# Performance work log

Measured on AMD Instinct MI355X. Metric: run time of the kernel, lower is better.

## Reference

```python
import jax, jax.numpy as jnp
import numpy as np

ALPHA = 1.0
NEG = -1e20  # boundary value used by the torch module


def _compute_mu(W, alpha):
    """DTW location parameter mu: [B, Na+1, Nb+1].
    mu[i,j] = alpha*W[i-1,j-1] + logsumexp(mu[i-1,j], mu[i,j-1], mu[i-1,j-1]).
    Row-wise scan (outer over i) with an inner scan over j for the
    left-dependency; fully vectorized over batch.
    """
    B, Na, Nb = W.shape
    aW = alpha * W  # [B, Na, Nb]
    # row 0: mu[:,0,0]=0, mu[:,0,1:]=-1e20
    row0 = jnp.concatenate([jnp.zeros((B, 1), W.dtype),
                            jnp.full((B, Nb), NEG, W.dtype)], axis=1)

    def row_step(prev_row, w_row):  # prev_row [B, Nb+1], w_row [B, Nb]
        up = prev_row[:, 1:]    # mu[i-1, j]   for j=1..Nb -> [B, Nb]
        diag = prev_row[:, :-1]  # mu[i-1, j-1]            -> [B, Nb]

        def col_step(left, inp):
            u, d, w = inp  # each [B]
            val = w + jax.nn.logsumexp(jnp.stack([u, left, d], axis=0), axis=0)
            return val, val

        left0 = jnp.full((B,), NEG, W.dtype)  # mu[i, 0] = -1e20
        xs = (up.T, diag.T, w_row.T)          # scan over Nb
        _, vals = jax.lax.scan(col_step, left0, xs)  # [Nb, B]
        new_row = jnp.concatenate([jnp.full((B, 1), NEG, W.dtype), vals.T], axis=1)
        return new_row, new_row

    _, rows = jax.lax.scan(row_step, row0, jnp.swapaxes(aW, 0, 1))  # [Na, B, Nb+1]
    mu = jnp.concatenate([row0[:, None, :], jnp.swapaxes(rows, 0, 1)], axis=1)
    return mu  # [B, Na+1, Nb+1]


def _compute_pi(W, mu, mask, alpha):
    """Reduced transition tensor pi: [B, Na, Nb, 3] (softmax over moves)."""
    up = mu[:, :-1, 1:]    # mu[i-1, j]
    left = mu[:, 1:, :-1]  # mu[i, j-1]
    diag = mu[:, :-1, :-1]  # mu[i-1, j-1]
    raw = jnp.stack([up, left, diag], axis=-1) + alpha * W[..., None]
    return jax.nn.softmax(raw, axis=-1) * mask


def setup_inputs() -> dict:
    key = jax.random.key(0)
    k1, _ = jax.random.split(key)
    B, Na, Nb = 64, 384, 384
    W = jax.random.normal(k1, (B, Na, Nb), dtype=jnp.float32)
    mask = jnp.ones((B, Na, Nb, 1), dtype=jnp.float32)
    return {"W": W, "mask": mask}


def reference(W, mask):
    mu = _compute_mu(W, ALPHA)
    pi = _compute_pi(W, mu, mask, ALPHA)
    return (mu, pi)
```

## Files before the change

### kernel.cpp

```cpp
#include <hip/hip_runtime.h>

#define NA 384
#define NB 384
#define NBATCH 64
#define NEGV -1e20f
#define C 8
#define NCW 6
#define TOT_CH 56
#define WPITCH 68
#define LOG2E 1.44269504088896340736f
#define LN2   0.69314718055994530942f

typedef float f4 __attribute__((ext_vector_type(4)));

struct alignas(16) SharedT {
    float stage[2][NCW][64 * 9];
    float wtile[4][NCW][8 * WPITCH];
    float bound[NCW - 1][NB + 1];
    int   progress[NCW - 1];
    int   computed[NCW];
    int   drained[NCW][2];
    int   wready[NCW];
};

__device__ __forceinline__ void loadW8(const float* __restrict__ Wb, int rbase,
                                       int kk, int l, float (&r)[8])
{
    const int rl = l >> 3, cc = l & 7;
    const int colb = 8 * kk + cc;
#pragma unroll
    for (int i = 0; i < 8; ++i) {
        const int row = 8 * i + rl;
        int col = colb - row;
        col = col < 0 ? 0 : (col > NB - 1 ? NB - 1 : col);
        r[i] = Wb[(size_t)(rbase + row) * NB + col];
    }
}

__device__ __forceinline__ void writeWt(float* __restrict__ wt,
                                        const float (&r)[8], int l) {
#pragma unroll
    for (int i = 0; i < 8; ++i) wt[i * WPITCH + l] = r[i];
}

__device__ __forceinline__ void readWc(const float* __restrict__ wt, int l,
                                       float (&wc)[8]) {
    const int wb = (l >> 3) * WPITCH + (l & 7) * 8;
    const f4 lo = *(const f4*)(wt + wb);
    const f4 hi = *(const f4*)(wt + wb + 4);
    wc[0] = lo.x * LOG2E; wc[1] = lo.y * LOG2E;
    wc[2] = lo.z * LOG2E; wc[3] = lo.w * LOG2E;
    wc[4] = hi.x * LOG2E; wc[5] = hi.y * LOG2E;
    wc[6] = hi.z * LOG2E; wc[7] = hi.w * LOG2E;
}

template<bool FULL>
__device__ __forceinline__ void chunk_body(int k, int w, int l,
        float (&wc)[8], float& val, float& diag, SharedT& sh)
{
    const int s0 = 1 + k * C;

    if (k >= 2) {
        volatile int* dr = &sh.drained[w][k & 1];
        while (*dr < k - 2) __builtin_amdgcn_s_sleep(1);
        __builtin_amdgcn_sched_barrier(0);
        asm volatile("" ::: "memory");
    }
    if (w > 0 && s0 <= NB) {
        const int need = (s0 + C - 1 < NB) ? s0 + C - 1 : NB;
        volatile int* pr = &sh.progress[w - 1];
        while (*pr < need) { }
        __builtin_amdgcn_sched_barrier(0);
        asm volatile("" ::: "memory");
    }
    float bnd[C];
    if (w > 0) {
#pragma unroll
        for (int c = 0; c < C; ++c) {
            const int s = s0 + c;
            bnd[c] = sh.bound[w - 1][s <= NB ? s : NB];
        }
    }

    float* st = &sh.stage[k & 1][w][0];
    __builtin_amdgcn_s_setprio(1);
#pragma unroll
    for (int c = 0; c < C; ++c) {
        const int s = s0 + c;
        float upv = __int_as_float(__builtin_amdgcn_update_dpp(
            0, __float_as_int(val), 0x138 , 0xF, 0xF, false));
        if (l == 0) upv = (w > 0 && s <= NB) ? bnd[c] : NEGV;
        const int j = s - l;
        if (FULL || (j >= 1 && j <= NB)) {
            const float m  = fmaxf(fmaxf(upv, val), diag);
            const float eu = exp2f(upv  - m);
            const float el = exp2f(val  - m);
            const float ed = exp2f(diag - m);
            const float nv = wc[c] + m + __log2f(eu + el + ed);
            st[l * 9 + c] = nv;
            if (w < NCW - 1 && l == 63) sh.bound[w][j] = nv;
            diag = upv;
            val  = nv;
        }
    }
    asm volatile("s_waitcnt lgkmcnt(0)" ::: "memory");
    if (l == 63) {
        if (w < NCW - 1) {
            const int done = s0 + C - 1 - 63;
            if (done >= 1) *(volatile int*)&sh.progress[w] = done;
        }
        *(volatile int*)&sh.computed[w] = k + 1;
    }
    __builtin_amdgcn_s_setprio(0);

    if (k + 1 < TOT_CH) {
        volatile int* wr = &sh.wready[w];
        while (*wr < k + 2) { }
        __builtin_amdgcn_sched_barrier(0);
        asm volatile("" ::: "memory");
        readWc(&sh.wtile[(k + 1) & 3][w][0], l, wc);
    }
}

template<bool FULL>
__device__ __forceinline__ void io_iter(int k, int cw, int l,
        const float* __restrict__ Wb, int rbase, float* __restrict__ mub,
        float (&wreg)[8], SharedT& sh)
{
    volatile int* cp = &sh.computed[cw];
    while (*cp < k + 1) __builtin_amdgcn_s_sleep(1);
    __builtin_amdgcn_sched_barrier(0);
    asm volatile("" ::: "memory");

    const float* st = &sh.stage[k & 1][cw][0];
    float v[8];
    const int lr = l >> 3, cc = l & 7;
#pragma unroll
    for (int q = 0; q < 8; ++q) v[q] = st[(lr + 8 * q) * 9 + cc];
    asm volatile("s_waitcnt lgkmcnt(0)" ::: "memory");
    if (l == 0) *(volatile int*)&sh.drained[cw][k & 1] = k;

    if (k + 3 < TOT_CH) {
        writeWt(&sh.wtile[(k + 3) & 3][cw][0], wreg, l);
        asm volatile("s_waitcnt lgkmcnt(0)" ::: "memory");
        if (l == 0) *(volatile int*)&sh.wready[cw] = k + 4;
        if (k + 5 < TOT_CH) loadW8(Wb, rbase, k + 5, l, wreg);
    }

    const int colbase = k * C;
#pragma unroll
    for (int q = 0; q < 8; ++q) {
        const int lrow = lr + 8 * q;
        const int col  = colbase + cc - lrow;
        if (FULL || (col >= 0 && col < NB))
            mub[(size_t)(rbase + lrow + 1) * (NB + 1) + col + 1] = v[q] * LN2;
    }
}

__global__ __launch_bounds__(768, 1) void dtw_mu(const float* __restrict__ W,
                                                 float* __restrict__ mu)
{
    __shared__ SharedT sh;
    const int b = blockIdx.x, tid = threadIdx.x;
    const int w = tid >> 6, l = tid & 63;
    const float* Wb = W + (size_t)b * NA * NB;
    float* mub = mu + (size_t)b * (NA + 1) * (NB + 1);

    if (tid < 384) {
        mub[tid + 1] = NEGV;
        mub[(size_t)(tid + 1) * (NB + 1)] = NEGV;
    }
    if (tid == 0) mub[0] = 0.0f;
    if (tid < NCW - 1) sh.progress[tid] = 0;
    if (tid < NCW) { sh.computed[tid] = 0; sh.wready[tid] = 0; }
    if (tid < 2 * NCW) sh.drained[tid >> 1][tid & 1] = -1;
    __syncthreads();

    if (w < NCW) {
        const int rbase = w << 6;
        float val  = NEGV;
        float diag = (rbase + l == 0) ? 0.0f : NEGV;
        float wc[8];
        {
            volatile int* wr = &sh.wready[w];
            while (*wr < 1) { }
            __builtin_amdgcn_sched_barrier(0);
            asm volatile("" ::: "memory");
            readWc(&sh.wtile[0][w][0], l, wc);
        }
        for (int k = 0; k < 8; ++k)       chunk_body<false>(k, w, l, wc, val, diag, sh);
        for (int k = 8; k < 48; ++k)      chunk_body<true >(k, w, l, wc, val, diag, sh);
        for (int k = 48; k < TOT_CH; ++k) chunk_body<false>(k, w, l, wc, val, diag, sh);
    } else {
        const int cw = w - NCW, rbase = cw << 6;
        float r0[8], r1[8], r2[8], rA[8], rB[8];
        loadW8(Wb, rbase, 0, l, r0);
        loadW8(Wb, rbase, 1, l, r1);
        loadW8(Wb, rbase, 2, l, r2);
        loadW8(Wb, rbase, 3, l, rA);
        loadW8(Wb, rbase, 4, l, rB);
        writeWt(&sh.wtile[0][cw][0], r0, l);
        writeWt(&sh.wtile[1][cw][0], r1, l);
        writeWt(&sh.wtile[2][cw][0], r2, l);
        asm volatile("s_waitcnt lgkmcnt(0)" ::: "memory");
        if (l == 0) *(volatile int*)&sh.wready[cw] = 3;

        for (int k = 0; k < 8; k += 2) {
            io_iter<false>(k,     cw, l, Wb, rbase, mub, rA, sh);
            io_iter<false>(k + 1, cw, l, Wb, rbase, mub, rB, sh);
        }
        for (int k = 8; k < 48; k += 2) {
            io_iter<true >(k,     cw, l, Wb, rbase, mub, rA, sh);
            io_iter<true >(k + 1, cw, l, Wb, rbase, mub, rB, sh);
        }
        for (int k = 48; k < TOT_CH; k += 2) {
            io_iter<false>(k,     cw, l, Wb, rbase, mub, rA, sh);
            io_iter<false>(k + 1, cw, l, Wb, rbase, mub, rB, sh);
        }
    }
}

__global__ __launch_bounds__(256) void dtw_pi(const float* __restrict__ W,
        const float* __restrict__ mask, const float* __restrict__ mu,
        float* __restrict__ pi)
{
    const long long idx = ((long long)blockIdx.x * 256 + threadIdx.x) * 4;
    const int rr = (int)(idx / NB);
    const int jj = (int)(idx - (long long)rr * NB);
    const int b  = rr / NA;
    const int ii = rr - b * NA;
    const float* m0 = mu + (size_t)b * (NA + 1) * (NB + 1)
                         + (size_t)ii * (NB + 1) + jj;
    const float* m1 = m0 + (NB + 1);
    const float d0 = m0[0], d1 = m0[1], d2 = m0[2], d3 = m0[3], d4 = m0[4];
    const float L0 = m1[0], L1 = m1[1], L2 = m1[2], L3 = m1[3], L4 = m1[4];
    const f4 wv = *(const f4*)(W + idx);
    const f4 mk = *(const f4*)(mask + idx);

    const float t0 = wv.x - L1, t1 = wv.y - L2, t2 = wv.z - L3, t3 = wv.w - L4;
    f4 o0, o1, o2;
    o0.x = exp2f((d1 + t0) * LOG2E) * mk.x;
    o0.y = exp2f((L0 + t0) * LOG2E) * mk.x;
    o0.z = exp2f((d0 + t0) * LOG2E) * mk.x;
    o0.w = exp2f((d2 + t1) * LOG2E) * mk.y;
    o1.x = exp2f((L1 + t1) * LOG2E) * mk.y;
    o1.y = exp2f((d1 + t1) * LOG2E) * mk.y;
    o1.z = exp2f((d3 + t2) * LOG2E) * mk.z;
    o1.w = exp2f((L2 + t2) * LOG2E) * mk.z;
    o2.x = exp2f((d2 + t2) * LOG2E) * mk.z;
    o2.y = exp2f((d4 + t3) * LOG2E) * mk.w;
    o2.z = exp2f((L3 + t3) * LOG2E) * mk.w;
    o2.w = exp2f((d3 + t3) * LOG2E) * mk.w;

    f4* po = (f4*)(pi + idx * 3);
    po[0] = o0; po[1] = o1; po[2] = o2;
}

extern "C" void kernel_launch(void* const* d_in, const int* in_sizes, int n_in,
                              void* d_out, int out_size, void* d_ws, size_t ws_size,
                              hipStream_t stream) {
    const float* W    = (const float*)d_in[0];
    const float* mask = (const float*)d_in[1];
    float* mu = (float*)d_out;
    float* pi = mu + (size_t)NBATCH * (NA + 1) * (NB + 1);

    hipLaunchKernelGGL(dtw_mu, dim3(NBATCH), dim3(768), 0, stream, W, mu);

    const int cells  = NBATCH * NA * NB;
    const int blocks = cells / (256 * 4);
    hipLaunchKernelGGL(dtw_pi, dim3(blocks), dim3(256), 0, stream,
                       W, mask, mu, pi);
}
```

Before: 167.0 us.

## Split each batch's DTW wavefront across four blocks with global-memory edge handoff

The mu recurrence for each batch is now spread over 4 blocks of 256 threads instead of one 768-thread block. Each block holds two compute waves, each owning a 48-row band, plus two IO waves. Band boundaries inside a block still pass through shared memory. Boundaries between blocks pass through tagged 64-bit atomics in a scratch area carved from the pi output, with the next chunk's boundary values prefetched ahead of use. The goal is to use more CUs and cut per-CU contention. In exchange it adds cross-block spin-waits through L2, relies on all blocks being resident at once, and leaves a quarter of the lanes idle in each compute wave.

```diff
diff --git a/kernel.cpp b/kernel.cpp
--- a/kernel.cpp
+++ b/kernel.cpp
@@ -5,47 +5,51 @@
 #define NBATCH 64
 #define NEGV -1e20f
 #define C 8
-#define NCW 6
-#define TOT_CH 56
+#define TOT_CH 54
+#define RPW 48
+#define NBLK 4
 #define WPITCH 68
 #define LOG2E 1.44269504088896340736f
 #define LN2   0.69314718055994530942f
+#define MUP (NB + 1)
 
 typedef float f4 __attribute__((ext_vector_type(4)));
+typedef unsigned long long u64;
 
 struct alignas(16) SharedT {
-    float stage[2][NCW][64 * 9];
-    float wtile[4][NCW][8 * WPITCH];
-    float bound[NCW - 1][NB + 1];
-    int   progress[NCW - 1];
-    int   computed[NCW];
-    int   drained[NCW][2];
-    int   wready[NCW];
+    float stage[2][2][RPW * 9];
+    float wtile[4][2][6 * WPITCH];
+    float bound[NB + 1];
+    int   progress;
+    int   computed[2];
+    int   drained[2][2];
+    int   wready[2];
 };
 
-__device__ __forceinline__ void loadW8(const float* __restrict__ Wb, int rbase,
-                                       int kk, int l, float (&r)[8])
+__device__ __forceinline__ void loadW6(const float* __restrict__ Wb, int wrow0,
+                                       int kk, int l, float (&r)[6])
 {
     const int rl = l >> 3, cc = l & 7;
     const int colb = 8 * kk + cc;
 #pragma unroll
-    for (int i = 0; i < 8; ++i) {
+    for (int i = 0; i < 6; ++i) {
         const int row = 8 * i + rl;
         int col = colb - row;
         col = col < 0 ? 0 : (col > NB - 1 ? NB - 1 : col);
-        r[i] = Wb[(size_t)(rbase + row) * NB + col];
-    }
-}
-
-__device__ __forceinline__ void writeWt(float* __restrict__ wt,
-                                        const float (&r)[8], int l) {
-#pragma unroll
-    for (int i = 0; i < 8; ++i) wt[i * WPITCH + l] = r[i];
+        r[i] = Wb[(size_t)(wrow0 + row) * NB + col];
+    }
+}
+
+__device__ __forceinline__ void writeWt6(float* __restrict__ wt,
+                                         const float (&r)[6], int l) {
+#pragma unroll
+    for (int i = 0; i < 6; ++i) wt[i * WPITCH + l] = r[i];
 }
 
 __device__ __forceinline__ void readWc(const float* __restrict__ wt, int l,
                                        float (&wc)[8]) {
-    const int wb = (l >> 3) * WPITCH + (l & 7) * 8;
+    const int ll = l < RPW ? l : RPW - 1;
+    const int wb = (ll >> 3) * WPITCH + (ll & 7) * 8;
     const f4 lo = *(const f4*)(wt + wb);
     const f4 hi = *(const f4*)(wt + wb + 4);
     wc[0] = lo.x * LOG2E; wc[1] = lo.y * LOG2E;
@@ -54,168 +58,244 @@
     wc[6] = hi.z * LOG2E; wc[7] = hi.w * LOG2E;
 }
 
-template<bool FULL>
-__device__ __forceinline__ void chunk_body(int k, int w, int l,
-        float (&wc)[8], float& val, float& diag, SharedT& sh)
+__device__ __forceinline__ u64 packbv(int j, float v) {
+    return ((u64)(unsigned)j << 32) | (u64)__float_as_uint(v);
+}
+
+template<int EIN, int EOUT, bool FULL>
+__device__ __forceinline__ void chunk_body(int k, int r, int l,
+        float (&wc)[8], float (&bnd)[8], u64 (&pkN)[8],
+        float& val, float& diag, SharedT& sh,
+        u64* __restrict__ gOut, const u64* __restrict__ gIn)
 {
     const int s0 = 1 + k * C;
-
-    if (k >= 2) {
-        volatile int* dr = &sh.drained[w][k & 1];
-        while (*dr < k - 2) __builtin_amdgcn_s_sleep(1);
-        __builtin_amdgcn_sched_barrier(0);
-        asm volatile("" ::: "memory");
-    }
-    if (w > 0 && s0 <= NB) {
-        const int need = (s0 + C - 1 < NB) ? s0 + C - 1 : NB;
-        volatile int* pr = &sh.progress[w - 1];
-        while (*pr < need) { }
-        __builtin_amdgcn_sched_barrier(0);
-        asm volatile("" ::: "memory");
-    }
-    float bnd[C];
-    if (w > 0) {
-#pragma unroll
-        for (int c = 0; c < C; ++c) {
-            const int s = s0 + c;
-            bnd[c] = sh.bound[w - 1][s <= NB ? s : NB];
-        }
-    }
-
-    float* st = &sh.stage[k & 1][w][0];
+    float* st = &sh.stage[k & 1][r][0];
+
+    if (EIN == 2) {
+        bool ok;
+        do {
+            ok = true;
+#pragma unroll
+            for (int c = 0; c < C; ++c) {
+                const int s = s0 + c;
+                if (s <= NB) ok = ok && ((int)(pkN[c] >> 32) == s);
+            }
+            if (!ok) {
+#pragma unroll
+                for (int c = 0; c < C; ++c) {
+                    const int s = s0 + c;
+                    if (s <= NB)
+                        pkN[c] = __hip_atomic_load(gIn + s, __ATOMIC_RELAXED,
+                                                   __HIP_MEMORY_SCOPE_AGENT);
+                }
+            }
+        } while (!ok);
+#pragma unroll
+        for (int c = 0; c < C; ++c) bnd[c] = __uint_as_float((unsigned)pkN[c]);
+        if (k + 1 < TOT_CH && s0 + C <= NB) {
+#pragma unroll
+            for (int c = 0; c < C; ++c) {
+                const int s = s0 + C + c;
+                if (s <= NB)
+                    pkN[c] = __hip_atomic_load(gIn + s, __ATOMIC_RELAXED,
+                                               __HIP_MEMORY_SCOPE_AGENT);
+            }
+        }
+    }
+
     __builtin_amdgcn_s_setprio(1);
 #pragma unroll
     for (int c = 0; c < C; ++c) {
         const int s = s0 + c;
         float upv = __int_as_float(__builtin_amdgcn_update_dpp(
             0, __float_as_int(val), 0x138 , 0xF, 0xF, false));
-        if (l == 0) upv = (w > 0 && s <= NB) ? bnd[c] : NEGV;
+        if (l == 0) upv = (EIN != 0 && s <= NB) ? bnd[c] : NEGV;
         const int j = s - l;
-        if (FULL || (j >= 1 && j <= NB)) {
+        if ((FULL && l < RPW) || (!FULL && l < RPW && j >= 1 && j <= NB)) {
             const float m  = fmaxf(fmaxf(upv, val), diag);
             const float eu = exp2f(upv  - m);
             const float el = exp2f(val  - m);
             const float ed = exp2f(diag - m);
             const float nv = wc[c] + m + __log2f(eu + el + ed);
             st[l * 9 + c] = nv;
-            if (w < NCW - 1 && l == 63) sh.bound[w][j] = nv;
+            if (EOUT == 1 && l == RPW - 1) sh.bound[j] = nv;
+            if (EOUT == 2 && l == RPW - 1)
+                __hip_atomic_store(gOut + j, packbv(j, nv), __ATOMIC_RELAXED,
+                                   __HIP_MEMORY_SCOPE_AGENT);
             diag = upv;
             val  = nv;
         }
     }
     asm volatile("s_waitcnt lgkmcnt(0)" ::: "memory");
-    if (l == 63) {
-        if (w < NCW - 1) {
-            const int done = s0 + C - 1 - 63;
-            if (done >= 1) *(volatile int*)&sh.progress[w] = done;
-        }
-        *(volatile int*)&sh.computed[w] = k + 1;
+    if (l == RPW - 1) {
+        if (EOUT == 1) {
+            const int done = s0 + C - 1 - (RPW - 1);
+            if (done >= 1) *(volatile int*)&sh.progress = done;
+        }
+        *(volatile int*)&sh.computed[r] = k + 1;
     }
     __builtin_amdgcn_s_setprio(0);
 
     if (k + 1 < TOT_CH) {
-        volatile int* wr = &sh.wready[w];
+        volatile int* wr = &sh.wready[r];
         while (*wr < k + 2) { }
         __builtin_amdgcn_sched_barrier(0);
         asm volatile("" ::: "memory");
-        readWc(&sh.wtile[(k + 1) & 3][w][0], l, wc);
-    }
+        readWc(&sh.wtile[(k + 1) & 3][r][0], l, wc);
+
+        volatile int* dr = &sh.drained[r][(k + 1) & 1];
+        while (*dr < k - 1) __builtin_amdgcn_s_sleep(1);
+        __builtin_amdgcn_sched_barrier(0);
+        asm volatile("" ::: "memory");
+
+        if (EIN == 1 && s0 + C <= NB) {
+            int need = 8 * k + 16; need = need > NB ? NB : need;
+            volatile int* pr = &sh.progress;
+            while (*pr < need) { }
+            __builtin_amdgcn_sched_barrier(0);
+            asm volatile("" ::: "memory");
+#pragma unroll
+            for (int c = 0; c < C; ++c) {
+                int s = s0 + C + c; s = s > NB ? NB : s;
+                bnd[c] = sh.bound[s];
+            }
+        }
+    }
+}
+
+template<int EIN, int EOUT>
+__device__ __forceinline__ void relay_run(int r, int l, SharedT& sh, int rb48,
+        u64* __restrict__ gOut, const u64* __restrict__ gIn)
+{
+    float val  = NEGV;
+    float diag = (rb48 + l == 0) ? 0.0f : NEGV;
+    float wc[8], bnd[8];
+    u64 pkN[8];
+
+    {
+        volatile int* wr = &sh.wready[r];
+        while (*wr < 1) { }
+        __builtin_amdgcn_sched_barrier(0);
+        asm volatile("" ::: "memory");
+        readWc(&sh.wtile[0][r][0], l, wc);
+    }
+    if (EIN == 1) {
+        volatile int* pr = &sh.progress;
+        while (*pr < C) { }
+        __builtin_amdgcn_sched_barrier(0);
+        asm volatile("" ::: "memory");
+#pragma unroll
+        for (int c = 0; c < C; ++c) bnd[c] = sh.bound[1 + c];
+    }
+    if (EIN == 2) {
+#pragma unroll
+        for (int c = 0; c < C; ++c)
+            pkN[c] = __hip_atomic_load(gIn + 1 + c, __ATOMIC_RELAXED,
+                                       __HIP_MEMORY_SCOPE_AGENT);
+    }
+
+    for (int k = 0; k < 6; ++k)
+        chunk_body<EIN, EOUT, false>(k, r, l, wc, bnd, pkN, val, diag, sh, gOut, gIn);
+    for (int k = 6; k < 48; ++k)
+        chunk_body<EIN, EOUT, true >(k, r, l, wc, bnd, pkN, val, diag, sh, gOut, gIn);
+    for (int k = 48; k < TOT_CH; ++k)
+        chunk_body<EIN, EOUT, false>(k, r, l, wc, bnd, pkN, val, diag, sh, gOut, gIn);
 }
 
 template<bool FULL>
-__device__ __forceinline__ void io_iter(int k, int cw, int l,
-        const float* __restrict__ Wb, int rbase, float* __restrict__ mub,
-        float (&wreg)[8], SharedT& sh)
-{
-    volatile int* cp = &sh.computed[cw];
+__device__ __forceinline__ void io_iter(int k, int r, int l,
+        const float* __restrict__ Wb, int rb48, float* __restrict__ mub,
+        float (&wreg)[6], SharedT& sh)
+{
+    volatile int* cp = &sh.computed[r];
     while (*cp < k + 1) __builtin_amdgcn_s_sleep(1);
     __builtin_amdgcn_sched_barrier(0);
     asm volatile("" ::: "memory");
 
-    const float* st = &sh.stage[k & 1][cw][0];
-    float v[8];
+    const float* st = &sh.stage[k & 1][r][0];
     const int lr = l >> 3, cc = l & 7;
-#pragma unroll
-    for (int q = 0; q < 8; ++q) v[q] = st[(lr + 8 * q) * 9 + cc];
+    float v[6];
+#pragma unroll
+    for (int qq = 0; qq < 6; ++qq) v[qq] = st[(lr + 8 * qq) * 9 + cc];
     asm volatile("s_waitcnt lgkmcnt(0)" ::: "memory");
-    if (l == 0) *(volatile int*)&sh.drained[cw][k & 1] = k;
+    if (l == 0) *(volatile int*)&sh.drained[r][k & 1] = k;
 
     if (k + 3 < TOT_CH) {
-        writeWt(&sh.wtile[(k + 3) & 3][cw][0], wreg, l);
+        writeWt6(&sh.wtile[(k + 3) & 3][r][0], wreg, l);
         asm volatile("s_waitcnt lgkmcnt(0)" ::: "memory");
-        if (l == 0) *(volatile int*)&sh.wready[cw] = k + 4;
-        if (k + 5 < TOT_CH) loadW8(Wb, rbase, k + 5, l, wreg);
+        if (l == 0) *(volatile int*)&sh.wready[r] = k + 4;
+        if (k + 5 < TOT_CH) loadW6(Wb, rb48, k + 5, l, wreg);
     }
 
     const int colbase = k * C;
 #pragma unroll
-    for (int q = 0; q < 8; ++q) {
-        const int lrow = lr + 8 * q;
-        const int col  = colbase + cc - lrow;
-        if (FULL || (col >= 0 && col < NB))
-            mub[(size_t)(rbase + lrow + 1) * (NB + 1) + col + 1] = v[q] * LN2;
-    }
-}
-
-__global__ __launch_bounds__(768, 1) void dtw_mu(const float* __restrict__ W,
-                                                 float* __restrict__ mu)
+    for (int qq = 0; qq < 6; ++qq) {
+        const int row = lr + 8 * qq;
+        const int col = colbase + cc - row;
+        if (FULL || (unsigned)col < (unsigned)NB)
+            mub[(size_t)(rb48 + row + 1) * MUP + col + 1] = v[qq] * LN2;
+    }
+}
+
+__global__ __launch_bounds__(256) void dtw_mu(const float* __restrict__ W,
+                                              float* __restrict__ mu)
 {
     __shared__ SharedT sh;
-    const int b = blockIdx.x, tid = threadIdx.x;
+    const int bid = blockIdx.x;
+    const int b = bid & 63, q = bid >> 6;
+    const int tid = threadIdx.x;
     const int w = tid >> 6, l = tid & 63;
+
     const float* Wb = W + (size_t)b * NA * NB;
-    float* mub = mu + (size_t)b * (NA + 1) * (NB + 1);
-
-    if (tid < 384) {
-        mub[tid + 1] = NEGV;
-        mub[(size_t)(tid + 1) * (NB + 1)] = NEGV;
-    }
-    if (tid == 0) mub[0] = 0.0f;
-    if (tid < NCW - 1) sh.progress[tid] = 0;
-    if (tid < NCW) { sh.computed[tid] = 0; sh.wready[tid] = 0; }
-    if (tid < 2 * NCW) sh.drained[tid >> 1][tid & 1] = -1;
+    float* mub = mu + (size_t)b * MUP * MUP;
+    u64* edge = (u64*)(mu + (size_t)NBATCH * MUP * MUP) + (size_t)b * 3 * 400;
+
+    if (q == 0)
+        for (int t = tid; t < MUP; t += 256) mub[t] = (t == 0) ? 0.0f : NEGV;
+    if (tid < 96) mub[(size_t)(96 * q + tid + 1) * MUP] = NEGV;
+    if (tid < 2) { sh.computed[tid] = 0; sh.wready[tid] = 0; }
+    if (tid < 4) sh.drained[tid >> 1][tid & 1] = -1;
+    if (tid == 0) sh.progress = 0;
     __syncthreads();
 
-    if (w < NCW) {
-        const int rbase = w << 6;
-        float val  = NEGV;
-        float diag = (rbase + l == 0) ? 0.0f : NEGV;
-        float wc[8];
-        {
-            volatile int* wr = &sh.wready[w];
-            while (*wr < 1) { }
-            __builtin_amdgcn_sched_barrier(0);
-            asm volatile("" ::: "memory");
-            readWc(&sh.wtile[0][w][0], l, wc);
-        }
-        for (int k = 0; k < 8; ++k)       chunk_body<false>(k, w, l, wc, val, diag, sh);
-        for (int k = 8; k < 48; ++k)      chunk_body<true >(k, w, l, wc, val, diag, sh);
-        for (int k = 48; k < TOT_CH; ++k) chunk_body<false>(k, w, l, wc, val, diag, sh);
+    if (w < 2) {
+        const int r = w;
+        const int rb48 = 96 * q + 48 * r;
+        if (r == 0) {
+            if (q == 0) relay_run<0, 1>(r, l, sh, rb48, nullptr, nullptr);
+            else        relay_run<2, 1>(r, l, sh, rb48, nullptr,
+                                        edge + (size_t)(q - 1) * 400);
+        } else {
+            if (q == NBLK - 1) relay_run<1, 0>(r, l, sh, rb48, nullptr, nullptr);
+            else               relay_run<1, 2>(r, l, sh, rb48,
+                                               edge + (size_t)q * 400, nullptr);
+        }
     } else {
-        const int cw = w - NCW, rbase = cw << 6;
-        float r0[8], r1[8], r2[8], rA[8], rB[8];
-        loadW8(Wb, rbase, 0, l, r0);
-        loadW8(Wb, rbase, 1, l, r1);
-        loadW8(Wb, rbase, 2, l, r2);
-        loadW8(Wb, rbase, 3, l, rA);
-        loadW8(Wb, rbase, 4, l, rB);
-        writeWt(&sh.wtile[0][cw][0], r0, l);
-        writeWt(&sh.wtile[1][cw][0], r1, l);
-        writeWt(&sh.wtile[2][cw][0], r2, l);
+        const int r = w - 2;
+        const int rb48 = 96 * q + 48 * r;
+        float f0[6], f1[6], f2[6], rA[6], rB[6];
+        loadW6(Wb, rb48, 0, l, f0);
+        loadW6(Wb, rb48, 1, l, f1);
+        loadW6(Wb, rb48, 2, l, f2);
+        loadW6(Wb, rb48, 3, l, rA);
+        loadW6(Wb, rb48, 4, l, rB);
+        writeWt6(&sh.wtile[0][r][0], f0, l);
+        writeWt6(&sh.wtile[1][r][0], f1, l);
+        writeWt6(&sh.wtile[2][r][0], f2, l);
         asm volatile("s_waitcnt lgkmcnt(0)" ::: "memory");
-        if (l == 0) *(volatile int*)&sh.wready[cw] = 3;
-
-        for (int k = 0; k < 8; k += 2) {
-            io_iter<false>(k,     cw, l, Wb, rbase, mub, rA, sh);
-            io_iter<false>(k + 1, cw, l, Wb, rbase, mub, rB, sh);
-        }
-        for (int k = 8; k < 48; k += 2) {
-            io_iter<true >(k,     cw, l, Wb, rbase, mub, rA, sh);
-            io_iter<true >(k + 1, cw, l, Wb, rbase, mub, rB, sh);
+        if (l == 0) *(volatile int*)&sh.wready[r] = 3;
+
+        for (int k = 0; k < 6; k += 2) {
+            io_iter<false>(k,     r, l, Wb, rb48, mub, rA, sh);
+            io_iter<false>(k + 1, r, l, Wb, rb48, mub, rB, sh);
+        }
+        for (int k = 6; k < 48; k += 2) {
+            io_iter<true >(k,     r, l, Wb, rb48, mub, rA, sh);
+            io_iter<true >(k + 1, r, l, Wb, rb48, mub, rB, sh);
         }
         for (int k = 48; k < TOT_CH; k += 2) {
-            io_iter<false>(k,     cw, l, Wb, rbase, mub, rA, sh);
-            io_iter<false>(k + 1, cw, l, Wb, rbase, mub, rB, sh);
+            io_iter<false>(k,     r, l, Wb, rb48, mub, rA, sh);
+            io_iter<false>(k + 1, r, l, Wb, rb48, mub, rB, sh);
         }
     }
 }
@@ -229,9 +309,8 @@
     const int jj = (int)(idx - (long long)rr * NB);
     const int b  = rr / NA;
     const int ii = rr - b * NA;
-    const float* m0 = mu + (size_t)b * (NA + 1) * (NB + 1)
-                         + (size_t)ii * (NB + 1) + jj;
-    const float* m1 = m0 + (NB + 1);
+    const float* m0 = mu + (size_t)b * MUP * MUP + (size_t)ii * MUP + jj;
+    const float* m1 = m0 + MUP;
     const float d0 = m0[0], d1 = m0[1], d2 = m0[2], d3 = m0[3], d4 = m0[4];
     const float L0 = m1[0], L1 = m1[1], L2 = m1[2], L3 = m1[3], L4 = m1[4];
     const f4 wv = *(const f4*)(W + idx);
@@ -262,9 +341,9 @@
     const float* W    = (const float*)d_in[0];
     const float* mask = (const float*)d_in[1];
     float* mu = (float*)d_out;
-    float* pi = mu + (size_t)NBATCH * (NA + 1) * (NB + 1);
-
-    hipLaunchKernelGGL(dtw_mu, dim3(NBATCH), dim3(768), 0, stream, W, mu);
+    float* pi = mu + (size_t)NBATCH * MUP * MUP;
+
+    hipLaunchKernelGGL(dtw_mu, dim3(NBATCH * NBLK), dim3(256), 0, stream, W, mu);
 
     const int cells  = NBATCH * NA * NB;
     const int blocks = cells / (256 * 4);
```

After: 196.1 us. +17.5%, slower.
